# Performance work log

Hardware: AMD Instinct MI355X
Metric: run time of the kernel (lower is better)

Reference implementation:

```python
import jax, jax.numpy as jnp
import numpy as np

NHEAD = 16
FREQ = 10000.0


def rope(x, freq=FREQ):
    # x: [B, S, D]; rotary applied over the FULL feature dim (pre head-split),
    # pairing even/odd channels, matching the original module's op order.
    B, S, D = x.shape
    inv_freq = freq ** (-jnp.arange(0, D, 2, dtype=jnp.float32) / D)  # [D/2]
    ang = jnp.arange(S, dtype=jnp.float32)[:, None] * inv_freq[None, :]  # [S, D/2]
    cos, sin = jnp.cos(ang), jnp.sin(ang)
    x1, x2 = x[..., 0::2], x[..., 1::2]
    out_even = x1 * cos - x2 * sin
    out_odd = x1 * sin + x2 * cos
    return jnp.stack([out_even, out_odd], axis=-1).reshape(B, S, D)


def setup_inputs() -> dict:
    key = jax.random.key(0)
    ks = jax.random.split(key, 9)
    B, S, D = 4, 2048, 1024
    sc = 1.0 / np.sqrt(D)
    return {
        "queries": jax.random.normal(ks[0], (B, S, D), jnp.float32),
        "Wq": jax.random.normal(ks[1], (D, D), jnp.float32) * sc,
        "bq": jnp.zeros((D,), jnp.float32),
        "Wk": jax.random.normal(ks[2], (D, D), jnp.float32) * sc,
        "bk": jnp.zeros((D,), jnp.float32),
        "Wv": jax.random.normal(ks[3], (D, D), jnp.float32) * sc,
        "bv": jnp.zeros((D,), jnp.float32),
        "Wo": jax.random.normal(ks[4], (D, D), jnp.float32) * sc,
        "bo": jnp.zeros((D,), jnp.float32),
    }


def reference(queries, Wq, bq, Wk, bk, Wv, bv, Wo, bo):
    B, S, D = queries.shape
    H = NHEAD
    dh = D // H
    # self-attention: values = keys = queries
    q = rope(queries @ Wq.T + bq)
    k = rope(queries @ Wk.T + bk)
    v = queries @ Wv.T + bv
    # separate heads: [B, S, D] -> [B, H, S, dh]
    q = q.reshape(B, S, H, dh).transpose(0, 2, 1, 3)
    k = k.reshape(B, S, H, dh).transpose(0, 2, 1, 3)
    v = v.reshape(B, S, H, dh).transpose(0, 2, 1, 3)
    scores = jnp.einsum("bhqd,bhkd->bhqk", q, k) / jnp.sqrt(jnp.float32(dh))
    attn = jax.nn.softmax(scores, axis=-1)
    heads = jnp.einsum("bhqk,bhkd->bhqd", attn, v)
    out = heads.transpose(0, 2, 1, 3).reshape(B, S, D)
    return out @ Wo.T + bo
```

## Files before the change

### kernel.cpp

```cpp
#include <hip/hip_runtime.h>
#include <stdint.h>

typedef __bf16 bf16_t;
typedef __bf16 bf16x4 __attribute__((ext_vector_type(4)));
typedef __bf16 bf16x8 __attribute__((ext_vector_type(8)));
typedef float  f32x4  __attribute__((ext_vector_type(4)));

#define BB   4
#define SS   2048
#define DD   1024
#define HH   16
#define DH   64

#if __has_builtin(__builtin_amdgcn_exp2f)
#define EXP2F(x) __builtin_amdgcn_exp2f(x)
#else
#define EXP2F(x) __expf((x) * 0.6931471805599453f)
#endif

__device__ __forceinline__ void gload_lds16(const void* g, void* l) {
    __builtin_amdgcn_global_load_lds(
        (__attribute__((address_space(1))) void*)(uintptr_t)g,
        (__attribute__((address_space(3))) void*)(uint32_t)(uintptr_t)l,
        16, 0, 0);
}

__global__ __launch_bounds__(256) void cvt_kernel(const float* __restrict__ src,
                                                  bf16_t* __restrict__ dst, int n4) {
    int i = blockIdx.x * 256 + threadIdx.x;
    if (i < n4) {
        float4 v = ((const float4*)src)[i];
        bf16x4 o;
        o.x = (bf16_t)v.x; o.y = (bf16_t)v.y; o.z = (bf16_t)v.z; o.w = (bf16_t)v.w;
        ((bf16x4*)dst)[i] = o;
    }
}

__global__ __launch_bounds__(256) void cvt_weights(const float* __restrict__ Wq,
                                                   const float* __restrict__ Wk,
                                                   const float* __restrict__ Wv,
                                                   const float* __restrict__ Wo,
                                                   bf16_t* __restrict__ Wqkv,
                                                   bf16_t* __restrict__ Wob) {
    int i = blockIdx.x * 256 + threadIdx.x;
    int which = i >> 18, p = i & 262143;
    const float* src = (which == 0) ? Wq : (which == 1) ? Wk : (which == 2) ? Wv : Wo;
    bf16_t* dst = (which < 3) ? (Wqkv + (long)which * 1048576) : Wob;
    float4 v = ((const float4*)src)[p];
    bf16x4 o;
    o.x = (bf16_t)v.x; o.y = (bf16_t)v.y; o.z = (bf16_t)v.z; o.w = (bf16_t)v.w;
    ((bf16x4*)dst)[p] = o;
}

__global__ __launch_bounds__(256) void pack_bias(const float* __restrict__ bq,
                                                 const float* __restrict__ bk,
                                                 const float* __restrict__ bv,
                                                 float* __restrict__ bqkv) {
    int i = blockIdx.x * 256 + threadIdx.x;
    if (i < 3072)
        bqkv[i] = (i < 1024) ? bq[i] : ((i < 2048) ? bk[i - 1024] : bv[i - 2048]);
}

__global__ __launch_bounds__(256) void rope_tab(float2* __restrict__ tab) {
    int i = blockIdx.x * 256 + threadIdx.x;
    int s = i >> 9, pr = i & 511;
    float inv = powf(10000.0f, -(float)(2 * pr) * (1.0f / 1024.0f));
    float c, sn;
    sincosf((float)s * inv, &sn, &c);
    tab[i] = make_float2(c, sn);
}

__global__ __launch_bounds__(256, 2) void gemm_qkv_rope(
        const bf16_t* __restrict__ A, const bf16_t* __restrict__ Bm,
        const float* __restrict__ bias, const float2* __restrict__ tab,
        bf16_t* __restrict__ Qb, bf16_t* __restrict__ Kb, bf16_t* __restrict__ Vtmp)
{
    __shared__ __attribute__((aligned(16))) bf16_t As[128 * 32];
    __shared__ __attribute__((aligned(16))) bf16_t Bs[128 * 32];
    const int t = threadIdx.x;
    const int lane = t & 63, w = t >> 6;
    const int wm = w >> 1, wn = w & 1;
    const int l15 = lane & 15, l4 = lane >> 4;
    const long rowA0 = (long)blockIdx.x * 128;
    const long rowB0 = (long)blockIdx.y * 128;
    const int K = 1024, N = 1024;

    const f32x4 vz = {0.f, 0.f, 0.f, 0.f};
    f32x4 acc[4][4];
#pragma unroll
    for (int i = 0; i < 4; ++i)
#pragma unroll
        for (int j = 0; j < 4; ++j) acc[i][j] = vz;

    for (int kk = 0; kk < K; kk += 32) {
        __syncthreads();
#pragma unroll
        for (int i = 0; i < 2; ++i) {
            const int cb = i * 256 + w * 64;
            const int c  = cb + lane;
            const int r  = c >> 2;
            const int ko = (c & 3) << 3;
            gload_lds16(A  + (rowA0 + r) * K + kk + ko, As + cb * 8);
            gload_lds16(Bm + (rowB0 + r) * K + kk + ko, Bs + cb * 8);
        }
        __syncthreads();
        bf16x8 af[4], bfr[4];
#pragma unroll
        for (int i = 0; i < 4; ++i)
            af[i] = *(const bf16x8*)(As + (wm * 64 + i * 16 + l15) * 32 + l4 * 8);
#pragma unroll
        for (int j = 0; j < 4; ++j)
            bfr[j] = *(const bf16x8*)(Bs + (wn * 64 + j * 16 + l15) * 32 + l4 * 8);
#pragma unroll
        for (int i = 0; i < 4; ++i)
#pragma unroll
            for (int j = 0; j < 4; ++j)
                acc[i][j] = __builtin_amdgcn_mfma_f32_16x16x32_bf16(af[i], bfr[j], acc[i][j], 0, 0, 0);
    }

    const long crow0 = rowA0 + wm * 64;
    const int  ccol0 = (int)rowB0 + wn * 64;
    const int  part  = blockIdx.y >> 3;

    if (part == 2) {
#pragma unroll
        for (int i = 0; i < 4; ++i) {
#pragma unroll
            for (int j = 0; j < 4; ++j) {
                const int col = ccol0 + j * 16 + l15;
                const float bb = bias[col];
                const int vc = col - 2048;
#pragma unroll
                for (int r = 0; r < 4; ++r) {
                    const long row = crow0 + i * 16 + l4 * 4 + r;
                    Vtmp[row * N + vc] = (bf16_t)(acc[i][j][r] + bb);
                }
            }
        }
    } else {
        bf16_t* dst0 = part ? Kb : Qb;
        const int h = (ccol0 & 1023) >> 6;
#pragma unroll
        for (int i = 0; i < 4; ++i) {
#pragma unroll
            for (int j = 0; j < 4; ++j) {
                const int col = ccol0 + j * 16 + l15;
                const float bb = bias[col];
                const int even = !(col & 1);
                const int dd = j * 16 + l15;
                const float2* trow = tab + (col >> 1 & 511);
#pragma unroll
                for (int r = 0; r < 4; ++r) {
                    const long row = crow0 + i * 16 + l4 * 4 + r;
                    const int b = (int)(row >> 11), s = (int)(row & 2047);
                    const float val = acc[i][j][r] + bb;
                    const float par = __shfl_xor(val, 1);
                    const float2 cs = trow[s * 512];
                    const float out = even ? (val * cs.x - par * cs.y)
                                           : fmaf(val, cs.x, par * cs.y);
                    dst0[((long)((b * HH + h) * SS + s)) * DH + dd] = (bf16_t)out;
                }
            }
        }
    }
}

template <int OUT_BF16>
__global__ __launch_bounds__(256, 2) void gemm_bt(
        const bf16_t* __restrict__ A, const bf16_t* __restrict__ Bm,
        const float* __restrict__ bias, void* __restrict__ Cout,
        int M, int N, int K)
{
    __shared__ __attribute__((aligned(16))) bf16_t As[128 * 32];
    __shared__ __attribute__((aligned(16))) bf16_t Bs[128 * 32];
    const int t = threadIdx.x;
    const int lane = t & 63, w = t >> 6;
    const int wm = w >> 1, wn = w & 1;
    const int l15 = lane & 15, l4 = lane >> 4;
    const long rowA0 = (long)blockIdx.x * 128;
    const long rowB0 = (long)blockIdx.y * 128;

    const f32x4 vz = {0.f, 0.f, 0.f, 0.f};
    f32x4 acc[4][4];
#pragma unroll
    for (int i = 0; i < 4; ++i)
#pragma unroll
        for (int j = 0; j < 4; ++j) acc[i][j] = vz;

    for (int kk = 0; kk < K; kk += 32) {
        __syncthreads();
#pragma unroll
        for (int i = 0; i < 2; ++i) {
            const int cb = i * 256 + w * 64;
            const int c  = cb + lane;
            const int r  = c >> 2;
            const int ko = (c & 3) << 3;
            gload_lds16(A  + (rowA0 + r) * K + kk + ko, As + cb * 8);
            gload_lds16(Bm + (rowB0 + r) * K + kk + ko, Bs + cb * 8);
        }
        __syncthreads();
        bf16x8 af[4], bfr[4];
#pragma unroll
        for (int i = 0; i < 4; ++i)
            af[i] = *(const bf16x8*)(As + (wm * 64 + i * 16 + l15) * 32 + l4 * 8);
#pragma unroll
        for (int j = 0; j < 4; ++j)
            bfr[j] = *(const bf16x8*)(Bs + (wn * 64 + j * 16 + l15) * 32 + l4 * 8);
#pragma unroll
        for (int i = 0; i < 4; ++i)
#pragma unroll
            for (int j = 0; j < 4; ++j)
                acc[i][j] = __builtin_amdgcn_mfma_f32_16x16x32_bf16(af[i], bfr[j], acc[i][j], 0, 0, 0);
    }

    const long crow0 = rowA0 + wm * 64;
    const int  ccol0 = (int)rowB0 + wn * 64;
#pragma unroll
    for (int i = 0; i < 4; ++i) {
#pragma unroll
        for (int j = 0; j < 4; ++j) {
            const int col = ccol0 + j * 16 + l15;
            const float bb = bias[col];
#pragma unroll
            for (int r = 0; r < 4; ++r) {
                const long row = crow0 + i * 16 + l4 * 4 + r;
                const float v = acc[i][j][r] + bb;
                if (OUT_BF16) ((bf16_t*)Cout)[row * N + col] = (bf16_t)v;
                else          ((float*)Cout)[row * N + col]  = v;
            }
        }
    }
}

__global__ __launch_bounds__(256) void repack_v(const bf16_t* __restrict__ Vtmp,
                                                bf16_t* __restrict__ Vt)
{
    __shared__ bf16_t tile[64][65];
    const int t = threadIdx.x;
    const int st = blockIdx.x, bh = blockIdx.y;
    const int b = bh >> 4, h = bh & 15;
    const long nbase = (long)b * SS + st * 64;
#pragma unroll
    for (int e = 0; e < 16; ++e) {
        const int i = e * 256 + t;
        const int r = i >> 6, d = i & 63;
        tile[r][d] = Vtmp[(nbase + r) * 1024 + h * 64 + d];
    }
    __syncthreads();
#pragma unroll
    for (int e = 0; e < 16; ++e) {
        const int i = e * 256 + t;
        const int d = i >> 6, s = i & 63;
        Vt[((long)bh * DH + d) * SS + st * 64 + s] = tile[s][d];
    }
}

__global__ __launch_bounds__(256, 4) void attn_kernel(const bf16_t* __restrict__ Qb,
                                                      const bf16_t* __restrict__ Kb,
                                                      const bf16_t* __restrict__ Vt,
                                                      bf16_t* __restrict__ Ob)
{
    __shared__ __attribute__((aligned(16))) bf16_t Ks[64 * 64];
    __shared__ __attribute__((aligned(16))) bf16_t Vs[64 * 64];
    __shared__ __attribute__((aligned(16))) bf16_t Ps[128 * 72];
    const int t = threadIdx.x, lane = t & 63, w = t >> 6;
    const int l15 = lane & 15, l4 = lane >> 4;
    const int xr = l15 & 7;
    const int qt = blockIdx.x, bh = blockIdx.y;
    const bf16_t* Qbh = Qb + (long)bh * SS * DH;
    const bf16_t* Kbh = Kb + (long)bh * SS * DH;
    const bf16_t* Vbh = Vt + (long)bh * DH * SS;

    const int qbase = qt * 128 + w * 32;
    bf16x8 qf[2][2];
#pragma unroll
    for (int s = 0; s < 2; ++s) {
        const long qrow = qbase + 16 * s + l15;
        qf[s][0] = *(const bf16x8*)(Qbh + qrow * DH + l4 * 8);
        qf[s][1] = *(const bf16x8*)(Qbh + qrow * DH + 32 + l4 * 8);
    }

    const f32x4 vz = {0.f, 0.f, 0.f, 0.f};
    f32x4 oacc[2][4];
#pragma unroll
    for (int s = 0; s < 2; ++s)
#pragma unroll
        for (int j = 0; j < 4; ++j) oacc[s][j] = vz;
    float l_sum[2] = {0.f, 0.f};

    int srow[2], scc[2];
#pragma unroll
    for (int i = 0; i < 2; ++i) {
        const int L = i * 256 + w * 64 + lane;
        srow[i] = L >> 3;
        scc[i]  = (L & 7) ^ (srow[i] & 7);
    }

    const float SC = 0.125f * 1.4426950408889634f;
    const float BI = -8.0f  * 1.4426950408889634f;

    for (int kt = 0; kt < SS / 64; ++kt) {
        __syncthreads();
        const bf16_t* Ksrc = Kbh + (long)kt * 64 * DH;
#pragma unroll
        for (int i = 0; i < 2; ++i) {
            const int cb = i * 256 + w * 64;
            gload_lds16(Ksrc + srow[i] * 64 + scc[i] * 8, Ks + cb * 8);
            gload_lds16(Vbh + (long)srow[i] * SS + kt * 64 + scc[i] * 8, Vs + cb * 8);
        }
        __syncthreads();

        f32x4 sacc[2][4];
#pragma unroll
        for (int s = 0; s < 2; ++s)
#pragma unroll
            for (int j = 0; j < 4; ++j) sacc[s][j] = vz;
#pragma unroll
        for (int j = 0; j < 4; ++j) {
            const int rk = (j * 16 + l15) * 64;
            const bf16x8 kf0 = *(const bf16x8*)(Ks + rk + ((l4 ^ xr) * 8));
            const bf16x8 kf1 = *(const bf16x8*)(Ks + rk + (((4 + l4) ^ xr) * 8));
#pragma unroll
            for (int s = 0; s < 2; ++s) {
                sacc[s][j] = __builtin_amdgcn_mfma_f32_16x16x32_bf16(kf0, qf[s][0], sacc[s][j], 0, 0, 0);
                sacc[s][j] = __builtin_amdgcn_mfma_f32_16x16x32_bf16(kf1, qf[s][1], sacc[s][j], 0, 0, 0);
            }
        }

#pragma unroll
        for (int s = 0; s < 2; ++s) {
#pragma unroll
            for (int j = 0; j < 4; ++j) {
                const float p0 = EXP2F(fmaf(sacc[s][j][0], SC, BI));
                const float p1 = EXP2F(fmaf(sacc[s][j][1], SC, BI));
                const float p2 = EXP2F(fmaf(sacc[s][j][2], SC, BI));
                const float p3 = EXP2F(fmaf(sacc[s][j][3], SC, BI));
                l_sum[s] += (p0 + p1) + (p2 + p3);
                bf16x4 pk;
                pk.x = (bf16_t)p0; pk.y = (bf16_t)p1; pk.z = (bf16_t)p2; pk.w = (bf16_t)p3;
                *(bf16x4*)(Ps + (w * 32 + 16 * s + l15) * 72 + j * 16 + l4 * 4) = pk;
            }
        }

        bf16x8 pf[2][2];
#pragma unroll
        for (int s = 0; s < 2; ++s) {
            pf[s][0] = *(const bf16x8*)(Ps + (w * 32 + 16 * s + l15) * 72 + l4 * 8);
            pf[s][1] = *(const bf16x8*)(Ps + (w * 32 + 16 * s + l15) * 72 + 32 + l4 * 8);
        }
#pragma unroll
        for (int j = 0; j < 4; ++j) {
            const int rv = (j * 16 + l15) * 64;
            const bf16x8 vf0 = *(const bf16x8*)(Vs + rv + ((l4 ^ xr) * 8));
            const bf16x8 vf1 = *(const bf16x8*)(Vs + rv + (((4 + l4) ^ xr) * 8));
#pragma unroll
            for (int s = 0; s < 2; ++s) {
                oacc[s][j] = __builtin_amdgcn_mfma_f32_16x16x32_bf16(pf[s][0], vf0, oacc[s][j], 0, 0, 0);
                oacc[s][j] = __builtin_amdgcn_mfma_f32_16x16x32_bf16(pf[s][1], vf1, oacc[s][j], 0, 0, 0);
            }
        }
    }

    const int b = bh >> 4, h = bh & 15;
#pragma unroll
    for (int s = 0; s < 2; ++s) {
        float lt = l_sum[s];
        lt += __shfl_xor(lt, 16);
        lt += __shfl_xor(lt, 32);
        const float inv = 1.0f / lt;
        float invr[4];
#pragma unroll
        for (int r = 0; r < 4; ++r)
            invr[r] = __shfl(inv, l4 * 4 + r);
#pragma unroll
        for (int j = 0; j < 4; ++j) {
#pragma unroll
            for (int r = 0; r < 4; ++r) {
                const int row = qbase + 16 * s + l4 * 4 + r;
                const float v = oacc[s][j][r] * invr[r];
                Ob[((long)(b * SS + row)) * DD + h * DH + j * 16 + l15] = (bf16_t)v;
            }
        }
    }
}

extern "C" void kernel_launch(void* const* d_in, const int* in_sizes, int n_in,
                              void* d_out, int out_size, void* d_ws, size_t ws_size,
                              hipStream_t stream)
{
    const float* queries = (const float*)d_in[0];
    const float* Wq = (const float*)d_in[1];
    const float* bq = (const float*)d_in[2];
    const float* Wk = (const float*)d_in[3];
    const float* bk = (const float*)d_in[4];
    const float* Wv = (const float*)d_in[5];
    const float* bv = (const float*)d_in[6];
    const float* Wo = (const float*)d_in[7];
    const float* bo = (const float*)d_in[8];

    char* ws = (char*)d_ws;
    size_t off = 0;
    auto alloc = [&](size_t bytes) { size_t o = off; off += (bytes + 255) & ~(size_t)255; return o; };
    bf16_t* Xb   = (bf16_t*)(ws + alloc(8192u * 1024u * 2u));
    bf16_t* Wqkv = (bf16_t*)(ws + alloc(3072u * 1024u * 2u));
    bf16_t* Wob  = (bf16_t*)(ws + alloc(1024u * 1024u * 2u));
    float*  bqkv = (float*) (ws + alloc(3072u * 4u));
    float2* tab  = (float2*)(ws + alloc(2048u * 512u * 8u));
    bf16_t* Vtmp = (bf16_t*)(ws + alloc(8192u * 1024u * 2u));
    bf16_t* Qb   = (bf16_t*)(ws + alloc(64u * 2048u * 64u * 2u));
    bf16_t* Kb   = (bf16_t*)(ws + alloc(64u * 2048u * 64u * 2u));
    bf16_t* Vt   = (bf16_t*)(ws + alloc(64u * 64u * 2048u * 2u));
    bf16_t* Ob   = Xb;

    cvt_kernel<<<8192, 256, 0, stream>>>(queries, Xb, 2097152);
    cvt_weights<<<4096, 256, 0, stream>>>(Wq, Wk, Wv, Wo, Wqkv, Wob);
    pack_bias<<<12, 256, 0, stream>>>(bq, bk, bv, bqkv);
    rope_tab<<<4096, 256, 0, stream>>>(tab);

    gemm_qkv_rope<<<dim3(64, 24), 256, 0, stream>>>(Xb, Wqkv, bqkv, tab, Qb, Kb, Vtmp);
    repack_v<<<dim3(32, 64), 256, 0, stream>>>(Vtmp, Vt);
    attn_kernel<<<dim3(16, 64), 256, 0, stream>>>(Qb, Kb, Vt, Ob);
    gemm_bt<0><<<dim3(64, 8), 256, 0, stream>>>(Ob, Wob, bo, d_out, 8192, 1024, 1024);
}
```

Measured before the change: 310.8 us.

## Double-buffer K/V tiles in attention, vectorize V repack, merge prep kernels

The attention kernel now uses two LDS buffers for K and V, so the next tile's global-to-LDS loads are issued while the current tile is computed. This removes one barrier per iteration, and occupancy drops from 4 to 3 blocks per CU to make room for the extra LDS. The V transpose kernel now uses 16-byte vector loads and stores instead of scalar element copies. The four preprocessing kernels are merged into one launch to cut launch overhead. There is a risk that the async LDS loads are not guaranteed complete before use, because no wait or barrier sits between issuing stage kt+1 and reading buffer p in the next iteration other than the end-of-loop syncthreads.

After: 301.5 us. -3.0%, faster.

```diff
diff --git a/kernel.cpp b/kernel.cpp
--- a/kernel.cpp
+++ b/kernel.cpp
@@ -25,49 +25,44 @@
         16, 0, 0);
 }
 
-__global__ __launch_bounds__(256) void cvt_kernel(const float* __restrict__ src,
-                                                  bf16_t* __restrict__ dst, int n4) {
-    int i = blockIdx.x * 256 + threadIdx.x;
-    if (i < n4) {
-        float4 v = ((const float4*)src)[i];
+__global__ __launch_bounds__(256) void prep_kernel(
+        const float* __restrict__ queries,
+        const float* __restrict__ Wq, const float* __restrict__ Wk,
+        const float* __restrict__ Wv, const float* __restrict__ Wo,
+        const float* __restrict__ bq, const float* __restrict__ bk,
+        const float* __restrict__ bv,
+        bf16_t* __restrict__ Xb, bf16_t* __restrict__ Wqkv,
+        bf16_t* __restrict__ Wob, float* __restrict__ bqkv,
+        float2* __restrict__ tab)
+{
+    const int bid = blockIdx.x, t = threadIdx.x;
+    if (bid < 8192) {
+        const int i = bid * 256 + t;
+        float4 v = ((const float4*)queries)[i];
         bf16x4 o;
         o.x = (bf16_t)v.x; o.y = (bf16_t)v.y; o.z = (bf16_t)v.z; o.w = (bf16_t)v.w;
-        ((bf16x4*)dst)[i] = o;
-    }
-}
-
-__global__ __launch_bounds__(256) void cvt_weights(const float* __restrict__ Wq,
-                                                   const float* __restrict__ Wk,
-                                                   const float* __restrict__ Wv,
-                                                   const float* __restrict__ Wo,
-                                                   bf16_t* __restrict__ Wqkv,
-                                                   bf16_t* __restrict__ Wob) {
-    int i = blockIdx.x * 256 + threadIdx.x;
-    int which = i >> 18, p = i & 262143;
-    const float* src = (which == 0) ? Wq : (which == 1) ? Wk : (which == 2) ? Wv : Wo;
-    bf16_t* dst = (which < 3) ? (Wqkv + (long)which * 1048576) : Wob;
-    float4 v = ((const float4*)src)[p];
-    bf16x4 o;
-    o.x = (bf16_t)v.x; o.y = (bf16_t)v.y; o.z = (bf16_t)v.z; o.w = (bf16_t)v.w;
-    ((bf16x4*)dst)[p] = o;
-}
-
-__global__ __launch_bounds__(256) void pack_bias(const float* __restrict__ bq,
-                                                 const float* __restrict__ bk,
-                                                 const float* __restrict__ bv,
-                                                 float* __restrict__ bqkv) {
-    int i = blockIdx.x * 256 + threadIdx.x;
-    if (i < 3072)
-        bqkv[i] = (i < 1024) ? bq[i] : ((i < 2048) ? bk[i - 1024] : bv[i - 2048]);
-}
-
-__global__ __launch_bounds__(256) void rope_tab(float2* __restrict__ tab) {
-    int i = blockIdx.x * 256 + threadIdx.x;
-    int s = i >> 9, pr = i & 511;
-    float inv = powf(10000.0f, -(float)(2 * pr) * (1.0f / 1024.0f));
-    float c, sn;
-    sincosf((float)s * inv, &sn, &c);
-    tab[i] = make_float2(c, sn);
+        ((bf16x4*)Xb)[i] = o;
+    } else if (bid < 12288) {
+        const int i = (bid - 8192) * 256 + t;
+        const int which = i >> 18, p = i & 262143;
+        const float* src = (which == 0) ? Wq : (which == 1) ? Wk : (which == 2) ? Wv : Wo;
+        bf16_t* dst = (which < 3) ? (Wqkv + (long)which * 1048576) : Wob;
+        float4 v = ((const float4*)src)[p];
+        bf16x4 o;
+        o.x = (bf16_t)v.x; o.y = (bf16_t)v.y; o.z = (bf16_t)v.z; o.w = (bf16_t)v.w;
+        ((bf16x4*)dst)[p] = o;
+    } else if (bid < 16384) {
+        const int i = (bid - 12288) * 256 + t;
+        const int s = i >> 9, pr = i & 511;
+        float inv = powf(10000.0f, -(float)(2 * pr) * (1.0f / 1024.0f));
+        float c, sn;
+        sincosf((float)s * inv, &sn, &c);
+        tab[i] = make_float2(c, sn);
+    } else {
+        const int i = (bid - 16384) * 256 + t;
+        if (i < 3072)
+            bqkv[i] = (i < 1024) ? bq[i] : ((i < 2048) ? bk[i - 1024] : bv[i - 2048]);
+    }
 }
 
 __global__ __launch_bounds__(256, 2) void gemm_qkv_rope(
@@ -235,33 +230,39 @@
 __global__ __launch_bounds__(256) void repack_v(const bf16_t* __restrict__ Vtmp,
                                                 bf16_t* __restrict__ Vt)
 {
-    __shared__ bf16_t tile[64][65];
+    __shared__ bf16_t tile[64][66];
     const int t = threadIdx.x;
     const int st = blockIdx.x, bh = blockIdx.y;
     const int b = bh >> 4, h = bh & 15;
     const long nbase = (long)b * SS + st * 64;
-#pragma unroll
-    for (int e = 0; e < 16; ++e) {
-        const int i = e * 256 + t;
-        const int r = i >> 6, d = i & 63;
-        tile[r][d] = Vtmp[(nbase + r) * 1024 + h * 64 + d];
+    const int rr = t >> 3, c8 = (t & 7) * 8;
+#pragma unroll
+    for (int e = 0; e < 2; ++e) {
+        const int r = e * 32 + rr;
+        union { bf16x8 v; unsigned int u[4]; } ld;
+        ld.v = *(const bf16x8*)(Vtmp + (nbase + r) * 1024 + h * 64 + c8);
+#pragma unroll
+        for (int k = 0; k < 4; ++k)
+            *(unsigned int*)(&tile[r][c8 + 2 * k]) = ld.u[k];
     }
     __syncthreads();
 #pragma unroll
-    for (int e = 0; e < 16; ++e) {
-        const int i = e * 256 + t;
-        const int d = i >> 6, s = i & 63;
-        Vt[((long)bh * DH + d) * SS + st * 64 + s] = tile[s][d];
-    }
-}
-
-__global__ __launch_bounds__(256, 4) void attn_kernel(const bf16_t* __restrict__ Qb,
+    for (int e = 0; e < 2; ++e) {
+        const int d = e * 32 + rr;
+        bf16x8 o;
+#pragma unroll
+        for (int k = 0; k < 8; ++k) o[k] = tile[c8 + k][d];
+        *(bf16x8*)(Vt + ((long)bh * DH + d) * SS + st * 64 + c8) = o;
+    }
+}
+
+__global__ __launch_bounds__(256, 3) void attn_kernel(const bf16_t* __restrict__ Qb,
                                                       const bf16_t* __restrict__ Kb,
                                                       const bf16_t* __restrict__ Vt,
                                                       bf16_t* __restrict__ Ob)
 {
-    __shared__ __attribute__((aligned(16))) bf16_t Ks[64 * 64];
-    __shared__ __attribute__((aligned(16))) bf16_t Vs[64 * 64];
+    __shared__ __attribute__((aligned(16))) bf16_t Ks[2][64 * 64];
+    __shared__ __attribute__((aligned(16))) bf16_t Vs[2][64 * 64];
     __shared__ __attribute__((aligned(16))) bf16_t Ps[128 * 72];
     const int t = threadIdx.x, lane = t & 63, w = t >> 6;
     const int l15 = lane & 15, l4 = lane >> 4;
@@ -299,16 +300,24 @@
     const float SC = 0.125f * 1.4426950408889634f;
     const float BI = -8.0f  * 1.4426950408889634f;
 
-    for (int kt = 0; kt < SS / 64; ++kt) {
-        __syncthreads();
+    auto stage = [&](int kt, int buf) {
         const bf16_t* Ksrc = Kbh + (long)kt * 64 * DH;
 #pragma unroll
         for (int i = 0; i < 2; ++i) {
             const int cb = i * 256 + w * 64;
-            gload_lds16(Ksrc + srow[i] * 64 + scc[i] * 8, Ks + cb * 8);
-            gload_lds16(Vbh + (long)srow[i] * SS + kt * 64 + scc[i] * 8, Vs + cb * 8);
-        }
-        __syncthreads();
+            gload_lds16(Ksrc + srow[i] * 64 + scc[i] * 8, &Ks[buf][cb * 8]);
+            gload_lds16(Vbh + (long)srow[i] * SS + kt * 64 + scc[i] * 8, &Vs[buf][cb * 8]);
+        }
+    };
+
+    stage(0, 0);
+    __syncthreads();
+
+    for (int kt = 0; kt < SS / 64; ++kt) {
+        const int p = kt & 1;
+        if (kt + 1 < SS / 64) stage(kt + 1, p ^ 1);
+        const bf16_t* KsP = Ks[p];
+        const bf16_t* VsP = Vs[p];
 
         f32x4 sacc[2][4];
 #pragma unroll
@@ -318,8 +327,8 @@
 #pragma unroll
         for (int j = 0; j < 4; ++j) {
             const int rk = (j * 16 + l15) * 64;
-            const bf16x8 kf0 = *(const bf16x8*)(Ks + rk + ((l4 ^ xr) * 8));
-            const bf16x8 kf1 = *(const bf16x8*)(Ks + rk + (((4 + l4) ^ xr) * 8));
+            const bf16x8 kf0 = *(const bf16x8*)(KsP + rk + ((l4 ^ xr) * 8));
+            const bf16x8 kf1 = *(const bf16x8*)(KsP + rk + (((4 + l4) ^ xr) * 8));
 #pragma unroll
             for (int s = 0; s < 2; ++s) {
                 sacc[s][j] = __builtin_amdgcn_mfma_f32_16x16x32_bf16(kf0, qf[s][0], sacc[s][j], 0, 0, 0);
@@ -351,14 +360,16 @@
 #pragma unroll
         for (int j = 0; j < 4; ++j) {
             const int rv = (j * 16 + l15) * 64;
-            const bf16x8 vf0 = *(const bf16x8*)(Vs + rv + ((l4 ^ xr) * 8));
-            const bf16x8 vf1 = *(const bf16x8*)(Vs + rv + (((4 + l4) ^ xr) * 8));
+            const bf16x8 vf0 = *(const bf16x8*)(VsP + rv + ((l4 ^ xr) * 8));
+            const bf16x8 vf1 = *(const bf16x8*)(VsP + rv + (((4 + l4) ^ xr) * 8));
 #pragma unroll
             for (int s = 0; s < 2; ++s) {
                 oacc[s][j] = __builtin_amdgcn_mfma_f32_16x16x32_bf16(pf[s][0], vf0, oacc[s][j], 0, 0, 0);
                 oacc[s][j] = __builtin_amdgcn_mfma_f32_16x16x32_bf16(pf[s][1], vf1, oacc[s][j], 0, 0, 0);
             }
         }
+
+        __syncthreads();
     }
 
     const int b = bh >> 4, h = bh & 15;
@@ -412,10 +423,8 @@
     bf16_t* Vt   = (bf16_t*)(ws + alloc(64u * 64u * 2048u * 2u));
     bf16_t* Ob   = Xb;
 
-    cvt_kernel<<<8192, 256, 0, stream>>>(queries, Xb, 2097152);
-    cvt_weights<<<4096, 256, 0, stream>>>(Wq, Wk, Wv, Wo, Wqkv, Wob);
-    pack_bias<<<12, 256, 0, stream>>>(bq, bk, bv, bqkv);
-    rope_tab<<<4096, 256, 0, stream>>>(tab);
+    prep_kernel<<<16396, 256, 0, stream>>>(queries, Wq, Wk, Wv, Wo, bq, bk, bv,
+                                           Xb, Wqkv, Wob, bqkv, tab);
 
     gemm_qkv_rope<<<dim3(64, 24), 256, 0, stream>>>(Xb, Wqkv, bqkv, tab, Qb, Kb, Vtmp);
     repack_v<<<dim3(32, 64), 256, 0, stream>>>(Vtmp, Vt);
```
